# Kernel optimization log

Hardware: AMD Instinct MI355X
Metric: run time of the kernel (lower is better)

The kernel has to match this reference:

```python
import jax, jax.numpy as jnp
import numpy as np

N_NODES = 100000
N_EDGES = 1000000
N_GRAPHS = 256
NUM_NODE_TYPES = 200
EMB_DIM = 64
HID_DIM = 32


def _gcn_conv(x, src, dst, W, b, n):
    """PyG GCNConv: x' = D^-1/2 (A+I) D^-1/2 (x W) + b. src/dst already include self-loops."""
    xw = x @ W  # [n, out]
    ones = jnp.ones(dst.shape, dtype=xw.dtype)
    deg = jax.ops.segment_sum(ones, dst, num_segments=n)  # in-degree incl. self-loop
    dinv = jnp.where(deg > 0, jax.lax.rsqrt(jnp.maximum(deg, 1e-12)), 0.0)
    norm = dinv[src] * dinv[dst]  # [E+n]
    msg = xw[src] * norm[:, None]  # gather + scale
    return jax.ops.segment_sum(msg, dst, num_segments=n) + b


def setup_inputs() -> dict:
    key = jax.random.key(0)
    ks = jax.random.split(key, 12)
    x = jax.random.randint(ks[0], (N_NODES, 1), 0, NUM_NODE_TYPES, dtype=jnp.int64)
    edge_index = jax.random.randint(ks[1], (2, N_EDGES), 0, N_NODES, dtype=jnp.int64)
    batch = jnp.sort(jax.random.randint(ks[2], (N_NODES,), 0, N_GRAPHS, dtype=jnp.int64))
    s = 0.05
    emb = jax.random.normal(ks[3], (NUM_NODE_TYPES, EMB_DIM), dtype=jnp.float32)
    W1 = jax.random.normal(ks[4], (EMB_DIM, HID_DIM), dtype=jnp.float32) * s
    b1 = jnp.zeros((HID_DIM,), dtype=jnp.float32)
    W2 = jax.random.normal(ks[5], (HID_DIM, HID_DIM), dtype=jnp.float32) * s
    b2 = jnp.zeros((HID_DIM,), dtype=jnp.float32)
    Wc1 = jax.random.normal(ks[6], (HID_DIM, 16), dtype=jnp.float32) * s
    bc1 = jnp.zeros((16,), dtype=jnp.float32)
    Wc2 = jax.random.normal(ks[7], (16, 1), dtype=jnp.float32) * s
    bc2 = jnp.zeros((1,), dtype=jnp.float32)
    return dict(x=x, edge_index=edge_index, batch=batch, emb=emb, W1=W1, b1=b1,
                W2=W2, b2=b2, Wc1=Wc1, bc1=bc1, Wc2=Wc2, bc2=bc2)


def reference(x, edge_index, batch, emb, W1, b1, W2, b2, Wc1, bc1, Wc2, bc2):
    n = x.shape[0]
    ids = x[:, 0]  # x.squeeze()
    loops = jnp.arange(n, dtype=edge_index.dtype)
    src = jnp.concatenate([edge_index[0], loops])
    dst = jnp.concatenate([edge_index[1], loops])

    h = emb[ids]  # [N, 64] embedding lookup
    h = jax.nn.relu(_gcn_conv(h, src, dst, W1, b1, n))
    h = jax.nn.relu(_gcn_conv(h, src, dst, W2, b2, n))

    # global_mean_pool over batch segments
    seg_sum = jax.ops.segment_sum(h, batch, num_segments=N_GRAPHS)
    counts = jax.ops.segment_sum(jnp.ones((n,), dtype=h.dtype), batch, num_segments=N_GRAPHS)
    pooled = seg_sum / jnp.maximum(counts, 1.0)[:, None]  # [B, 32]

    hc = jax.nn.relu(pooled @ Wc1 + bc1)
    return jax.nn.sigmoid(hc @ Wc2 + bc2)  # [B, 1]
```

## Files before the change

kernel.cpp:

```cpp
#include <hip/hip_runtime.h>
#include <hip/hip_fp16.h>
#include <math.h>

#define N_NODES   100000
#define N_EDGES   1000000
#define N_GRAPHS  256
#define NUM_TYPES 200
#define EMB       64
#define HID       32

#define BSHIFT    8
#define BSTRIDE   256
#define NBUCK     ((N_NODES + BSTRIDE - 1) / BSTRIDE)
#define EPB       4096
#define NBINBLK   ((N_EDGES + EPB - 1) / EPB)
#define MAXBE     4096
#define SRCBITS   17
#define SRCMASK   0x1FFFF


__global__ __launch_bounds__(256) void k_binA(const int* __restrict__ dst,
                                              int* __restrict__ counts) {
    __shared__ int cnt[NBUCK];
    int tid = threadIdx.x, k = blockIdx.x;
    for (int b = tid; b < NBUCK; b += 256) cnt[b] = 0;
    __syncthreads();
    int base = k * EPB;
    int n = min(EPB, N_EDGES - base);
    for (int t = tid; t < n; t += 256) atomicAdd(&cnt[dst[base + t] >> BSHIFT], 1);
    __syncthreads();
    for (int b = tid; b < NBUCK; b += 256) counts[k * NBUCK + b] = cnt[b];
}

__global__ __launch_bounds__(512) void k_misc(const int* __restrict__ counts,
                                              int* __restrict__ offs,
                                              int* __restrict__ bbase,
                                              const float* __restrict__ emb,
                                              const float* __restrict__ W1,
                                              float* __restrict__ table,
                                              float* __restrict__ pooled) {
    int tid = threadIdx.x;
    if (blockIdx.x == 0) {
        __shared__ int sA[512], sB[512];
        int total = 0;
        if (tid < NBUCK)
            for (int k = 0; k < NBINBLK; ++k) total += counts[k * NBUCK + tid];
        sA[tid] = (tid < NBUCK) ? total : 0;
        __syncthreads();
        int* in = sA; int* out = sB;
        for (int off = 1; off < 512; off <<= 1) {
            out[tid] = in[tid] + (tid >= off ? in[tid - off] : 0);
            __syncthreads();
            int* tmp = in; in = out; out = tmp;
        }
        int excl = in[tid] - ((tid < NBUCK) ? total : 0);
        if (tid < NBUCK) {
            bbase[tid] = excl;
            int run = excl;
            for (int k = 0; k < NBINBLK; ++k) {
                offs[k * NBUCK + tid] = run;
                run += counts[k * NBUCK + tid];
            }
        }
        if (tid == 0) bbase[NBUCK] = N_EDGES;
    } else if (blockIdx.x == 1) {
        for (int t = tid; t < NUM_TYPES * HID; t += 512) {
            int ty = t / HID, j = t % HID;
            float s = 0.f;
            for (int k = 0; k < EMB; ++k) s = fmaf(emb[ty * EMB + k], W1[k * HID + j], s);
            table[t] = s;
        }
    } else {
        for (int t = tid; t < N_GRAPHS * HID; t += 512) pooled[t] = 0.f;
    }
}

__global__ __launch_bounds__(256) void k_binB(const int* __restrict__ src,
                                              const int* __restrict__ dst,
                                              const int* __restrict__ offs,
                                              int* __restrict__ binned) {
    __shared__ int srcl[EPB];
    __shared__ int dstl[EPB];
    __shared__ unsigned short rank16[EPB];
    __shared__ unsigned short perm[EPB];
    __shared__ int cnt[NBUCK];
    __shared__ int loc[NBUCK];
    __shared__ int offsL[NBUCK];
    __shared__ int sA[512], sB[512];
    int tid = threadIdx.x, k = blockIdx.x;
    int base = k * EPB;
    int n = min(EPB, N_EDGES - base);
    for (int b = tid; b < NBUCK; b += 256) { cnt[b] = 0; offsL[b] = offs[k * NBUCK + b]; }
    __syncthreads();
    for (int t = tid; t < n; t += 256) {
        int s = src[base + t], d = dst[base + t];
        srcl[t] = s; dstl[t] = d;
        rank16[t] = (unsigned short)atomicAdd(&cnt[d >> BSHIFT], 1);
    }
    __syncthreads();
    for (int t = tid; t < 512; t += 256) sA[t] = (t < NBUCK) ? cnt[t] : 0;
    __syncthreads();
    int* in = sA; int* out = sB;
    for (int off = 1; off < 512; off <<= 1) {
        for (int t = tid; t < 512; t += 256)
            out[t] = in[t] + (t >= off ? in[t - off] : 0);
        __syncthreads();
        int* tmp = in; in = out; out = tmp;
    }
    for (int b = tid; b < NBUCK; b += 256) loc[b] = in[b] - cnt[b];
    __syncthreads();
    for (int t = tid; t < n; t += 256) {
        int b = dstl[t] >> BSHIFT;
        perm[loc[b] + rank16[t]] = (unsigned short)t;
    }
    __syncthreads();
    for (int t = tid; t < n; t += 256) {
        int e = perm[t];
        int d = dstl[e], b = d >> BSHIFT;
        int gpos = offsL[b] + (t - loc[b]);
        binned[gpos] = ((d & (BSTRIDE - 1)) << SRCBITS) | srcl[e];
    }
}

__global__ __launch_bounds__(256) void k_csr(const int* __restrict__ binned,
                                             const int* __restrict__ bbase,
                                             const int* __restrict__ ids,
                                             int* __restrict__ ssrc,
                                             int* __restrict__ row_ptr,
                                             float* __restrict__ dinv,
                                             int2* __restrict__ nodeinfo) {
    __shared__ int pk[MAXBE];
    __shared__ unsigned char dl[MAXBE];
    __shared__ unsigned short rank16[MAXBE];
    __shared__ unsigned short perm[MAXBE];
    __shared__ int degL[BSTRIDE];
    __shared__ int loc[BSTRIDE];
    __shared__ int sA[BSTRIDE], sB[BSTRIDE];
    int tid = threadIdx.x, b = blockIdx.x;
    int e0 = bbase[b], e1 = bbase[b + 1];
    int n = min(e1 - e0, MAXBE);
    degL[tid] = 0;
    __syncthreads();
    for (int t = tid; t < n; t += 256) {
        int v = binned[e0 + t];
        pk[t] = v;
        int d = v >> SRCBITS;
        dl[t] = (unsigned char)d;
        rank16[t] = (unsigned short)atomicAdd(&degL[d], 1);
    }
    __syncthreads();
    sA[tid] = degL[tid];
    __syncthreads();
    int* in = sA; int* out = sB;
    for (int off = 1; off < 256; off <<= 1) {
        out[tid] = in[tid] + (tid >= off ? in[tid - off] : 0);
        __syncthreads();
        int* tmp = in; in = out; out = tmp;
    }
    loc[tid] = in[tid] - degL[tid];
    __syncthreads();
    for (int t = tid; t < n; t += 256)
        perm[loc[dl[t]] + rank16[t]] = (unsigned short)t;
    __syncthreads();
    for (int t = tid; t < n; t += 256)
        ssrc[e0 + t] = pk[perm[t]] & SRCMASK;
    int i = b * BSTRIDE + tid;
    if (i < N_NODES) {
        row_ptr[i] = e0 + loc[tid];
        float dv = rsqrtf((float)degL[tid] + 1.0f);
        dinv[i] = dv;
        nodeinfo[i] = make_int2(ids[i], __float_as_int(dv));
    }
    if (b == NBUCK - 1 && tid == 0) row_ptr[N_NODES] = N_EDGES;
}

__global__ __launch_bounds__(256) void k_einfo(const int* __restrict__ ssrc,
                                               const int2* __restrict__ nodeinfo,
                                               unsigned int* __restrict__ einfo) {
    int e0 = (blockIdx.x * 256 + threadIdx.x) * 4;
    if (e0 >= N_EDGES) return;
    int4 s4 = *(const int4*)(ssrc + e0);
    int2 n0 = nodeinfo[s4.x], n1 = nodeinfo[s4.y];
    int2 n2 = nodeinfo[s4.z], n3 = nodeinfo[s4.w];
    uint4 r;
    r.x = ((unsigned)n0.x << 16) | __half_as_ushort(__float2half(__int_as_float(n0.y)));
    r.y = ((unsigned)n1.x << 16) | __half_as_ushort(__float2half(__int_as_float(n1.y)));
    r.z = ((unsigned)n2.x << 16) | __half_as_ushort(__float2half(__int_as_float(n2.y)));
    r.w = ((unsigned)n3.x << 16) | __half_as_ushort(__float2half(__int_as_float(n3.y)));
    *(uint4*)(einfo + e0) = r;
}


__global__ __launch_bounds__(256) void k_gather1(
        const int2* __restrict__ nodeinfo, const float* __restrict__ table,
        const int* __restrict__ row_ptr, const unsigned int* __restrict__ einfo,
        const float* __restrict__ b1, const float* __restrict__ W2,
        uint2* __restrict__ Y2h) {
    __shared__ float w[HID * HID];
    for (int k = threadIdx.x; k < HID * HID; k += 256) w[k] = W2[k];
    __syncthreads();

    int t = blockIdx.x * 256 + threadIdx.x;
    int i = t >> 3, p = t & 7;
    const float4* tab4 = (const float4*)table;

    int s0 = row_ptr[i], n = row_ptr[i + 1] - s0;
    int2 self = nodeinfo[i];
    float di = __int_as_float(self.y);
    float4 acc = tab4[self.x * 8 + p];
    acc.x *= di; acc.y *= di; acc.z *= di; acc.w *= di;

    for (int e = 0; e < n; e += 8) {
        unsigned int ei[8];
#pragma unroll
        for (int u = 0; u < 8; ++u) {
            int idx = e + u; idx = (idx > n - 1) ? n - 1 : idx;
            ei[u] = einfo[s0 + idx];
        }
#pragma unroll
        for (int u = 0; u < 8; ++u) {
            float ds = (e + u < n)
                ? __half2float(__ushort_as_half((unsigned short)(ei[u] & 0xFFFF))) : 0.f;
            float4 v = tab4[(ei[u] >> 16) * 8 + p];
            acc.x = fmaf(v.x, ds, acc.x);
            acc.y = fmaf(v.y, ds, acc.y);
            acc.z = fmaf(v.z, ds, acc.z);
            acc.w = fmaf(v.w, ds, acc.w);
        }
    }
    float4 bb = ((const float4*)b1)[p];
    float4 h;
    h.x = fmaxf(fmaf(di, acc.x, bb.x), 0.f);
    h.y = fmaxf(fmaf(di, acc.y, bb.y), 0.f);
    h.z = fmaxf(fmaf(di, acc.z, bb.z), 0.f);
    h.w = fmaxf(fmaf(di, acc.w, bb.w), 0.f);

    float o0 = 0.f, o1 = 0.f, o2 = 0.f, o3 = 0.f;
    const float4* w4 = (const float4*)w;
#pragma unroll
    for (int q = 0; q < 8; ++q) {
        float4 hq;
        hq.x = __shfl(h.x, q, 8);
        hq.y = __shfl(h.y, q, 8);
        hq.z = __shfl(h.z, q, 8);
        hq.w = __shfl(h.w, q, 8);
        float4 w0 = w4[(4 * q + 0) * 8 + p];
        float4 w1 = w4[(4 * q + 1) * 8 + p];
        float4 w2 = w4[(4 * q + 2) * 8 + p];
        float4 w3 = w4[(4 * q + 3) * 8 + p];
        o0 = fmaf(hq.x, w0.x, o0); o1 = fmaf(hq.x, w0.y, o1); o2 = fmaf(hq.x, w0.z, o2); o3 = fmaf(hq.x, w0.w, o3);
        o0 = fmaf(hq.y, w1.x, o0); o1 = fmaf(hq.y, w1.y, o1); o2 = fmaf(hq.y, w1.z, o2); o3 = fmaf(hq.y, w1.w, o3);
        o0 = fmaf(hq.z, w2.x, o0); o1 = fmaf(hq.z, w2.y, o1); o2 = fmaf(hq.z, w2.z, o2); o3 = fmaf(hq.z, w2.w, o3);
        o0 = fmaf(hq.w, w3.x, o0); o1 = fmaf(hq.w, w3.y, o1); o2 = fmaf(hq.w, w3.z, o2); o3 = fmaf(hq.w, w3.w, o3);
    }
    __half2 h01 = __halves2half2(__float2half(o0 * di), __float2half(o1 * di));
    __half2 h23 = __halves2half2(__float2half(o2 * di), __float2half(o3 * di));
    uint2 wv;
    wv.x = *(unsigned int*)&h01;
    wv.y = *(unsigned int*)&h23;
    Y2h[i * 8 + p] = wv;
}

__global__ __launch_bounds__(256) void k_gather2(
        const uint2* __restrict__ Y2h, const int* __restrict__ row_ptr,
        const int* __restrict__ ssrc, const float* __restrict__ dinv,
        const float* __restrict__ b2, const int* __restrict__ batch,
        float* __restrict__ pooled) {
    __shared__ float lp[32][HID];
    for (int k = threadIdx.x; k < 32 * HID; k += 256) ((float*)lp)[k] = 0.f;
    __syncthreads();

    int t = blockIdx.x * 256 + threadIdx.x;
    int i = t >> 3, p = t & 7;
    int i0 = (blockIdx.x * 256) >> 3;
    int gFirst = batch[i0];

    uint2 selfv = Y2h[i * 8 + p];
    float2 sa = __half22float2(*(__half2*)&selfv.x);
    float2 sb = __half22float2(*(__half2*)&selfv.y);
    float4 acc = make_float4(sa.x, sa.y, sb.x, sb.y);

    int s0 = row_ptr[i], n = row_ptr[i + 1] - s0;
    for (int e = 0; e < n; e += 8) {
        int ss[8];
#pragma unroll
        for (int u = 0; u < 8; ++u) {
            int idx = e + u; idx = (idx > n - 1) ? n - 1 : idx;
            ss[u] = ssrc[s0 + idx];
        }
        uint2 v[8];
#pragma unroll
        for (int u = 0; u < 8; ++u) v[u] = Y2h[ss[u] * 8 + p];
#pragma unroll
        for (int u = 0; u < 8; ++u) {
            float wg = (e + u < n) ? 1.f : 0.f;
            float2 fa = __half22float2(*(__half2*)&v[u].x);
            float2 fb = __half22float2(*(__half2*)&v[u].y);
            acc.x = fmaf(fa.x, wg, acc.x);
            acc.y = fmaf(fa.y, wg, acc.y);
            acc.z = fmaf(fb.x, wg, acc.z);
            acc.w = fmaf(fb.y, wg, acc.w);
        }
    }
    float di = dinv[i];
    float4 bb = ((const float4*)b2)[p];
    float4 h;
    h.x = fmaxf(fmaf(di, acc.x, bb.x), 0.f);
    h.y = fmaxf(fmaf(di, acc.y, bb.y), 0.f);
    h.z = fmaxf(fmaf(di, acc.z, bb.z), 0.f);
    h.w = fmaxf(fmaf(di, acc.w, bb.w), 0.f);

    int gl = batch[i] - gFirst;
    atomicAdd(&lp[gl][p * 4 + 0], h.x);
    atomicAdd(&lp[gl][p * 4 + 1], h.y);
    atomicAdd(&lp[gl][p * 4 + 2], h.z);
    atomicAdd(&lp[gl][p * 4 + 3], h.w);
    __syncthreads();

    int gLast = batch[i0 + 31];
    int ng = gLast - gFirst + 1;
    for (int k = threadIdx.x; k < ng * HID; k += 256) {
        float v = lp[k / HID][k % HID];
        if (v != 0.f) atomicAdd(&pooled[(gFirst + k / HID) * HID + (k % HID)], v);
    }
}

__global__ void k_head(const float* __restrict__ pooled, const int* __restrict__ batch,
                       const float* __restrict__ Wc1, const float* __restrict__ bc1,
                       const float* __restrict__ Wc2, const float* __restrict__ bc2,
                       float* __restrict__ out) {
    int g = blockIdx.x * blockDim.x + threadIdx.x;
    if (g >= N_GRAPHS) return;
    int lo = 0, hi = N_NODES;
    while (lo < hi) { int mid = (lo + hi) >> 1; if (batch[mid] < g) lo = mid + 1; else hi = mid; }
    int start = lo;
    hi = N_NODES;
    while (lo < hi) { int mid = (lo + hi) >> 1; if (batch[mid] < g + 1) lo = mid + 1; else hi = mid; }
    int end = lo;
    float inv = 1.0f / fmaxf((float)(end - start), 1.0f);
    float m[HID];
    for (int j = 0; j < HID; ++j) m[j] = pooled[g * HID + j] * inv;
    float hc[16];
    for (int j = 0; j < 16; ++j) {
        float s = bc1[j];
        for (int k = 0; k < HID; ++k) s = fmaf(m[k], Wc1[k * 16 + j], s);
        hc[j] = fmaxf(s, 0.f);
    }
    float s = bc2[0];
    for (int k = 0; k < 16; ++k) s = fmaf(hc[k], Wc2[k], s);
    out[g] = 1.0f / (1.0f + expf(-s));
}


extern "C" void kernel_launch(void* const* d_in, const int* in_sizes, int n_in,
                              void* d_out, int out_size, void* d_ws, size_t ws_size,
                              hipStream_t stream) {
    const int*   ids  = (const int*)d_in[0];
    const int*   src  = (const int*)d_in[1];
    const int*   dst  = ((const int*)d_in[1]) + N_EDGES;
    const int*   batch = (const int*)d_in[2];
    const float* emb  = (const float*)d_in[3];
    const float* W1   = (const float*)d_in[4];
    const float* b1   = (const float*)d_in[5];
    const float* W2   = (const float*)d_in[6];
    const float* b2   = (const float*)d_in[7];
    const float* Wc1  = (const float*)d_in[8];
    const float* bc1  = (const float*)d_in[9];
    const float* Wc2  = (const float*)d_in[10];
    const float* bc2  = (const float*)d_in[11];
    float* out = (float*)d_out;

    uint2* Y2h     = (uint2*)d_ws;
    int*   binned  = (int*)(Y2h + (size_t)N_NODES * 8);
    int*   ssrc    = binned + N_EDGES;
    unsigned int* einfo = (unsigned int*)(ssrc + N_EDGES);
    int2*  nodeinfo = (int2*)(einfo + N_EDGES);
    int*   counts  = (int*)(nodeinfo + N_NODES);
    int*   offs    = counts + NBINBLK * NBUCK;
    int*   bbase   = offs + NBINBLK * NBUCK;
    int*   row_ptr = bbase + NBUCK + 1;
    float* dinv    = (float*)(row_ptr + N_NODES + 2);
    float* table   = dinv + N_NODES;
    float* pooled  = table + NUM_TYPES * HID;

    const int B = 256;
    const int gNode8 = (N_NODES * 8) / B;

    k_binA<<<NBINBLK, B, 0, stream>>>(dst, counts);
    k_misc<<<3, 512, 0, stream>>>(counts, offs, bbase, emb, W1, table, pooled);
    k_binB<<<NBINBLK, B, 0, stream>>>(src, dst, offs, binned);
    k_csr<<<NBUCK, B, 0, stream>>>(binned, bbase, ids, ssrc, row_ptr, dinv, nodeinfo);
    k_einfo<<<(N_EDGES / 4 + B - 1) / B, B, 0, stream>>>(ssrc, nodeinfo, einfo);

    k_gather1<<<gNode8, B, 0, stream>>>(nodeinfo, table, row_ptr, einfo, b1, W2, Y2h);
    k_gather2<<<gNode8, B, 0, stream>>>((const uint2*)Y2h, row_ptr, ssrc, dinv, b2,
                                        batch, pooled);
    k_head<<<1, N_GRAPHS, 0, stream>>>(pooled, batch, Wc1, bc1, Wc2, bc2, out);
}
```

Baseline: 126.0 us.

## Fuse classifier head into gather2 via last-block flag; widen binning blocks

Removes the separate head kernel launch by having the last-finishing block of gather2, detected through an atomic counter reset in k_misc, compute the pooled-mean MLP head. The binB and csr kernels move from 256 to 512 threads per block, and their loops and scans are adjusted so each thread does less serial work. The workspace layout is recomputed with explicit offsets. The fused head adds a threadfence and an atomic per block, and the tail block does the head work serially after the last pooling atomics.

```diff
diff --git a/kernel.cpp b/kernel.cpp
--- a/kernel.cpp
+++ b/kernel.cpp
@@ -8,12 +8,11 @@
 #define NUM_TYPES 200
 #define EMB       64
 #define HID       32
-
 #define BSHIFT    8
 #define BSTRIDE   256
-#define NBUCK     ((N_NODES + BSTRIDE - 1) / BSTRIDE)
+#define NBUCK     391
 #define EPB       4096
-#define NBINBLK   ((N_EDGES + EPB - 1) / EPB)
+#define NCHUNK    245
 #define MAXBE     4096
 #define SRCBITS   17
 #define SRCMASK   0x1FFFF
@@ -38,26 +37,27 @@
                                               const float* __restrict__ emb,
                                               const float* __restrict__ W1,
                                               float* __restrict__ table,
-                                              float* __restrict__ pooled) {
+                                              float* __restrict__ pooled,
+                                              int* __restrict__ finish) {
     int tid = threadIdx.x;
     if (blockIdx.x == 0) {
         __shared__ int sA[512], sB[512];
         int total = 0;
         if (tid < NBUCK)
-            for (int k = 0; k < NBINBLK; ++k) total += counts[k * NBUCK + tid];
+            for (int k = 0; k < NCHUNK; ++k) total += counts[k * NBUCK + tid];
         sA[tid] = (tid < NBUCK) ? total : 0;
         __syncthreads();
-        int* in = sA; int* out = sB;
+        int* in = sA; int* ot = sB;
         for (int off = 1; off < 512; off <<= 1) {
-            out[tid] = in[tid] + (tid >= off ? in[tid - off] : 0);
+            ot[tid] = in[tid] + (tid >= off ? in[tid - off] : 0);
             __syncthreads();
-            int* tmp = in; in = out; out = tmp;
+            int* tmp = in; in = ot; ot = tmp;
         }
         int excl = in[tid] - ((tid < NBUCK) ? total : 0);
         if (tid < NBUCK) {
             bbase[tid] = excl;
             int run = excl;
-            for (int k = 0; k < NBINBLK; ++k) {
+            for (int k = 0; k < NCHUNK; ++k) {
                 offs[k * NBUCK + tid] = run;
                 run += counts[k * NBUCK + tid];
             }
@@ -72,10 +72,11 @@
         }
     } else {
         for (int t = tid; t < N_GRAPHS * HID; t += 512) pooled[t] = 0.f;
-    }
-}
-
-__global__ __launch_bounds__(256) void k_binB(const int* __restrict__ src,
+        if (tid == 0) *finish = 0;
+    }
+}
+
+__global__ __launch_bounds__(512) void k_binB(const int* __restrict__ src,
                                               const int* __restrict__ dst,
                                               const int* __restrict__ offs,
                                               int* __restrict__ binned) {
@@ -90,31 +91,30 @@
     int tid = threadIdx.x, k = blockIdx.x;
     int base = k * EPB;
     int n = min(EPB, N_EDGES - base);
-    for (int b = tid; b < NBUCK; b += 256) { cnt[b] = 0; offsL[b] = offs[k * NBUCK + b]; }
-    __syncthreads();
-    for (int t = tid; t < n; t += 256) {
+    if (tid < NBUCK) { cnt[tid] = 0; offsL[tid] = offs[k * NBUCK + tid]; }
+    __syncthreads();
+    for (int t = tid; t < n; t += 512) {
         int s = src[base + t], d = dst[base + t];
         srcl[t] = s; dstl[t] = d;
         rank16[t] = (unsigned short)atomicAdd(&cnt[d >> BSHIFT], 1);
     }
     __syncthreads();
-    for (int t = tid; t < 512; t += 256) sA[t] = (t < NBUCK) ? cnt[t] : 0;
-    __syncthreads();
-    int* in = sA; int* out = sB;
+    sA[tid] = (tid < NBUCK) ? cnt[tid] : 0;
+    __syncthreads();
+    int* in = sA; int* ot = sB;
     for (int off = 1; off < 512; off <<= 1) {
-        for (int t = tid; t < 512; t += 256)
-            out[t] = in[t] + (t >= off ? in[t - off] : 0);
+        ot[tid] = in[tid] + (tid >= off ? in[tid - off] : 0);
         __syncthreads();
-        int* tmp = in; in = out; out = tmp;
-    }
-    for (int b = tid; b < NBUCK; b += 256) loc[b] = in[b] - cnt[b];
-    __syncthreads();
-    for (int t = tid; t < n; t += 256) {
+        int* tmp = in; in = ot; ot = tmp;
+    }
+    if (tid < NBUCK) loc[tid] = in[tid] - cnt[tid];
+    __syncthreads();
+    for (int t = tid; t < n; t += 512) {
         int b = dstl[t] >> BSHIFT;
         perm[loc[b] + rank16[t]] = (unsigned short)t;
     }
     __syncthreads();
-    for (int t = tid; t < n; t += 256) {
+    for (int t = tid; t < n; t += 512) {
         int e = perm[t];
         int d = dstl[e], b = d >> BSHIFT;
         int gpos = offsL[b] + (t - loc[b]);
@@ -122,7 +122,7 @@
     }
 }
 
-__global__ __launch_bounds__(256) void k_csr(const int* __restrict__ binned,
+__global__ __launch_bounds__(512) void k_csr(const int* __restrict__ binned,
                                              const int* __restrict__ bbase,
                                              const int* __restrict__ ids,
                                              int* __restrict__ ssrc,
@@ -139,9 +139,9 @@
     int tid = threadIdx.x, b = blockIdx.x;
     int e0 = bbase[b], e1 = bbase[b + 1];
     int n = min(e1 - e0, MAXBE);
-    degL[tid] = 0;
-    __syncthreads();
-    for (int t = tid; t < n; t += 256) {
+    if (tid < BSTRIDE) degL[tid] = 0;
+    __syncthreads();
+    for (int t = tid; t < n; t += 512) {
         int v = binned[e0 + t];
         pk[t] = v;
         int d = v >> SRCBITS;
@@ -149,27 +149,29 @@
         rank16[t] = (unsigned short)atomicAdd(&degL[d], 1);
     }
     __syncthreads();
-    sA[tid] = degL[tid];
-    __syncthreads();
-    int* in = sA; int* out = sB;
-    for (int off = 1; off < 256; off <<= 1) {
-        out[tid] = in[tid] + (tid >= off ? in[tid - off] : 0);
+    if (tid < BSTRIDE) sA[tid] = degL[tid];
+    __syncthreads();
+    int* in = sA; int* ot = sB;
+    for (int off = 1; off < BSTRIDE; off <<= 1) {
+        if (tid < BSTRIDE) ot[tid] = in[tid] + (tid >= off ? in[tid - off] : 0);
         __syncthreads();
-        int* tmp = in; in = out; out = tmp;
-    }
-    loc[tid] = in[tid] - degL[tid];
-    __syncthreads();
-    for (int t = tid; t < n; t += 256)
+        int* tmp = in; in = ot; ot = tmp;
+    }
+    if (tid < BSTRIDE) loc[tid] = in[tid] - degL[tid];
+    __syncthreads();
+    for (int t = tid; t < n; t += 512)
         perm[loc[dl[t]] + rank16[t]] = (unsigned short)t;
     __syncthreads();
-    for (int t = tid; t < n; t += 256)
+    for (int t = tid; t < n; t += 512)
         ssrc[e0 + t] = pk[perm[t]] & SRCMASK;
-    int i = b * BSTRIDE + tid;
-    if (i < N_NODES) {
-        row_ptr[i] = e0 + loc[tid];
-        float dv = rsqrtf((float)degL[tid] + 1.0f);
-        dinv[i] = dv;
-        nodeinfo[i] = make_int2(ids[i], __float_as_int(dv));
+    if (tid < BSTRIDE) {
+        int i = b * BSTRIDE + tid;
+        if (i < N_NODES) {
+            row_ptr[i] = e0 + loc[tid];
+            float dv = rsqrtf((float)degL[tid] + 1.0f);
+            dinv[i] = dv;
+            nodeinfo[i] = make_int2(ids[i], __float_as_int(dv));
+        }
     }
     if (b == NBUCK - 1 && tid == 0) row_ptr[N_NODES] = N_EDGES;
 }
@@ -265,8 +267,12 @@
         const uint2* __restrict__ Y2h, const int* __restrict__ row_ptr,
         const int* __restrict__ ssrc, const float* __restrict__ dinv,
         const float* __restrict__ b2, const int* __restrict__ batch,
-        float* __restrict__ pooled) {
+        float* __restrict__ pooled, int* __restrict__ finish,
+        const float* __restrict__ Wc1, const float* __restrict__ bc1,
+        const float* __restrict__ Wc2, const float* __restrict__ bc2,
+        float* __restrict__ out) {
     __shared__ float lp[32][HID];
+    __shared__ int lastFlag;
     for (int k = threadIdx.x; k < 32 * HID; k += 256) ((float*)lp)[k] = 0.f;
     __syncthreads();
 
@@ -323,32 +329,37 @@
         float v = lp[k / HID][k % HID];
         if (v != 0.f) atomicAdd(&pooled[(gFirst + k / HID) * HID + (k % HID)], v);
     }
-}
-
-__global__ void k_head(const float* __restrict__ pooled, const int* __restrict__ batch,
-                       const float* __restrict__ Wc1, const float* __restrict__ bc1,
-                       const float* __restrict__ Wc2, const float* __restrict__ bc2,
-                       float* __restrict__ out) {
-    int g = blockIdx.x * blockDim.x + threadIdx.x;
-    if (g >= N_GRAPHS) return;
-    int lo = 0, hi = N_NODES;
-    while (lo < hi) { int mid = (lo + hi) >> 1; if (batch[mid] < g) lo = mid + 1; else hi = mid; }
-    int start = lo;
-    hi = N_NODES;
-    while (lo < hi) { int mid = (lo + hi) >> 1; if (batch[mid] < g + 1) lo = mid + 1; else hi = mid; }
-    int end = lo;
-    float inv = 1.0f / fmaxf((float)(end - start), 1.0f);
-    float m[HID];
-    for (int j = 0; j < HID; ++j) m[j] = pooled[g * HID + j] * inv;
-    float hc[16];
-    for (int j = 0; j < 16; ++j) {
-        float s = bc1[j];
-        for (int k = 0; k < HID; ++k) s = fmaf(m[k], Wc1[k * 16 + j], s);
-        hc[j] = fmaxf(s, 0.f);
-    }
-    float s = bc2[0];
-    for (int k = 0; k < 16; ++k) s = fmaf(hc[k], Wc2[k], s);
-    out[g] = 1.0f / (1.0f + expf(-s));
+    __syncthreads();
+
+    if (threadIdx.x == 0) {
+        __threadfence();
+        int d = __hip_atomic_fetch_add(finish, 1, __ATOMIC_ACQ_REL, __HIP_MEMORY_SCOPE_AGENT);
+        lastFlag = (d == (int)gridDim.x - 1);
+    }
+    __syncthreads();
+    if (lastFlag) {
+        int g = threadIdx.x;
+        int lo = 0, hi = N_NODES;
+        while (lo < hi) { int mid = (lo + hi) >> 1; if (batch[mid] < g) lo = mid + 1; else hi = mid; }
+        int start = lo;
+        hi = N_NODES;
+        while (lo < hi) { int mid = (lo + hi) >> 1; if (batch[mid] < g + 1) lo = mid + 1; else hi = mid; }
+        int end = lo;
+        float inv = 1.0f / fmaxf((float)(end - start), 1.0f);
+        float m[HID];
+        for (int j = 0; j < HID; ++j)
+            m[j] = __hip_atomic_load(&pooled[g * HID + j], __ATOMIC_RELAXED,
+                                     __HIP_MEMORY_SCOPE_AGENT) * inv;
+        float hc[16];
+        for (int j = 0; j < 16; ++j) {
+            float s = bc1[j];
+            for (int k = 0; k < HID; ++k) s = fmaf(m[k], Wc1[k * 16 + j], s);
+            hc[j] = fmaxf(s, 0.f);
+        }
+        float s = bc2[0];
+        for (int k = 0; k < 16; ++k) s = fmaf(hc[k], Wc2[k], s);
+        out[g] = 1.0f / (1.0f + expf(-s));
+    }
 }
 
 
@@ -370,30 +381,33 @@
     const float* bc2  = (const float*)d_in[11];
     float* out = (float*)d_out;
 
-    uint2* Y2h     = (uint2*)d_ws;
-    int*   binned  = (int*)(Y2h + (size_t)N_NODES * 8);
-    int*   ssrc    = binned + N_EDGES;
-    unsigned int* einfo = (unsigned int*)(ssrc + N_EDGES);
-    int2*  nodeinfo = (int2*)(einfo + N_EDGES);
-    int*   counts  = (int*)(nodeinfo + N_NODES);
-    int*   offs    = counts + NBINBLK * NBUCK;
-    int*   bbase   = offs + NBINBLK * NBUCK;
-    int*   row_ptr = bbase + NBUCK + 1;
-    float* dinv    = (float*)(row_ptr + N_NODES + 2);
-    float* table   = dinv + N_NODES;
-    float* pooled  = table + NUM_TYPES * HID;
+    int* W = (int*)d_ws;
+    size_t o = 0;
+    uint2* Y2h      = (uint2*)(W + o);        o += 1600000;
+    int*   binned   = W + o;                  o += N_EDGES;
+    int*   ssrc     = W + o;                  o += N_EDGES;
+    unsigned int* einfo = (unsigned int*)(W + o); o += N_EDGES;
+    int2*  nodeinfo = (int2*)(W + o);         o += 2 * N_NODES;
+    int*   counts   = W + o;                  o += NCHUNK * NBUCK;
+    int*   offs     = W + o;                  o += NCHUNK * NBUCK;
+    int*   bbase    = W + o;                  o += NBUCK + 1;
+    int*   row_ptr  = W + o;                  o += N_NODES + 1;
+    o = (o + 3) & ~(size_t)3;
+    float* dinv     = (float*)(W + o);        o += N_NODES;
+    float* table    = (float*)(W + o);        o += NUM_TYPES * HID;
+    float* pooled   = (float*)(W + o);        o += N_GRAPHS * HID;
+    int*   finish   = W + o;
 
     const int B = 256;
     const int gNode8 = (N_NODES * 8) / B;
 
-    k_binA<<<NBINBLK, B, 0, stream>>>(dst, counts);
-    k_misc<<<3, 512, 0, stream>>>(counts, offs, bbase, emb, W1, table, pooled);
-    k_binB<<<NBINBLK, B, 0, stream>>>(src, dst, offs, binned);
-    k_csr<<<NBUCK, B, 0, stream>>>(binned, bbase, ids, ssrc, row_ptr, dinv, nodeinfo);
+    k_binA<<<NCHUNK, B, 0, stream>>>(dst, counts);
+    k_misc<<<3, 512, 0, stream>>>(counts, offs, bbase, emb, W1, table, pooled, finish);
+    k_binB<<<NCHUNK, 512, 0, stream>>>(src, dst, offs, binned);
+    k_csr<<<NBUCK, 512, 0, stream>>>(binned, bbase, ids, ssrc, row_ptr, dinv, nodeinfo);
     k_einfo<<<(N_EDGES / 4 + B - 1) / B, B, 0, stream>>>(ssrc, nodeinfo, einfo);
 
     k_gather1<<<gNode8, B, 0, stream>>>(nodeinfo, table, row_ptr, einfo, b1, W2, Y2h);
     k_gather2<<<gNode8, B, 0, stream>>>((const uint2*)Y2h, row_ptr, ssrc, dinv, b2,
-                                        batch, pooled);
-    k_head<<<1, N_GRAPHS, 0, stream>>>(pooled, batch, Wc1, bc1, Wc2, bc2, out);
-}
+                                        batch, pooled, finish, Wc1, bc1, Wc2, bc2, out);
+}
```

After: 212.8 us. +68.9%, slower.
